# Performance work log

Measured on AMD Instinct MI355X. Metric: run time of the kernel, lower is better.

## Reference

```python
import jax, jax.numpy as jnp
import numpy as np

NUM_HEADS = 16
DIM_MODEL = 1024
DIM_K = DIM_MODEL // NUM_HEADS
B, S = 2, 2048


def _linear_params(key, d_in, d_out):
    kw, kb = jax.random.split(key)
    bound = 1.0 / np.sqrt(d_in)
    W = jax.random.uniform(kw, (d_out, d_in), jnp.float32, -bound, bound)
    b = jax.random.uniform(kb, (d_out,), jnp.float32, -bound, bound)
    return W, b


def setup_inputs() -> dict:
    key = jax.random.key(0)
    ks = jax.random.split(key, 7)
    Q_in = jax.random.normal(ks[0], (B, S, DIM_MODEL), jnp.float32)
    K_in = jax.random.normal(ks[1], (B, S, DIM_MODEL), jnp.float32)
    V_in = jax.random.normal(ks[2], (B, S, DIM_MODEL), jnp.float32)
    Wq, bq = _linear_params(ks[3], DIM_MODEL, DIM_MODEL)
    Wk, bk = _linear_params(ks[4], DIM_MODEL, DIM_MODEL)
    Wv, bv = _linear_params(ks[5], DIM_MODEL, DIM_MODEL)
    Wo, bo = _linear_params(ks[6], DIM_MODEL, DIM_MODEL)
    return {"Q_in": Q_in, "K_in": K_in, "V_in": V_in,
            "Wq": Wq, "bq": bq, "Wk": Wk, "bk": bk,
            "Wv": Wv, "bv": bv, "Wo": Wo, "bo": bo}


def reference(Q_in, K_in, V_in, Wq, bq, Wk, bk, Wv, bv, Wo, bo):
    # QKV projections (nn.Linear: x @ W.T + b)
    Q = Q_in @ Wq.T + bq
    K = K_in @ Wk.T + bk
    V = V_in @ Wv.T + bv
    # [B, S, D] -> [B, H, S, dk]
    def split_heads(x):
        return x.reshape(B, S, NUM_HEADS, DIM_K).transpose(0, 2, 1, 3)
    Qh, Kh, Vh = split_heads(Q), split_heads(K), split_heads(V)
    # Scaled dot-product attention
    scale = 1.0 / np.sqrt(DIM_K)
    scores = jnp.einsum('bhqd,bhkd->bhqk', Qh, Kh) * scale  # [B,H,S,S]
    attn = jax.nn.softmax(scores, axis=-1)
    out = jnp.einsum('bhqk,bhkd->bhqd', attn, Vh)  # [B,H,S,dk]
    # Merge heads -> [B, S, D]
    out = out.transpose(0, 2, 1, 3).reshape(B, S, DIM_MODEL)
    return out @ Wo.T + bo
```

## Files before the change

kernel.cpp:

```cpp
#include <hip/hip_runtime.h>
#include <stdint.h>

#define BB 2
#define SS 2048
#define DD 1024
#define HH 16
#define DKK 64
#define MT (BB*SS)

#define GSTRIDE 40

#define QSCALE 0.18033688011112042f

using short8  = __attribute__((ext_vector_type(8))) short;
using floatx4 = __attribute__((ext_vector_type(4))) float;
using u16x4   = __attribute__((ext_vector_type(4))) unsigned short;
typedef unsigned short u16;

__device__ __forceinline__ float ex2(float x) { return __builtin_amdgcn_exp2f(x); }

__device__ __forceinline__ u16 f2b(float f) {
  union { float f; unsigned u; } v; v.f = f;
  return (u16)((v.u + 0x7FFFu + ((v.u >> 16) & 1u)) >> 16);
}
__device__ __forceinline__ unsigned cvt_pk_bf16(float lo, float hi) {
  unsigned r;
  asm("v_cvt_pk_bf16_f32 %0, %1, %2" : "=v"(r) : "v"(lo), "v"(hi));
  return r;
}
__device__ __forceinline__ void pack16(const float4* p, short8& lo, short8& hi) {
  float4 x0 = p[0], x1 = p[1], x2 = p[2], x3 = p[3];
  lo[0]=(short)f2b(x0.x); lo[1]=(short)f2b(x0.y); lo[2]=(short)f2b(x0.z); lo[3]=(short)f2b(x0.w);
  lo[4]=(short)f2b(x1.x); lo[5]=(short)f2b(x1.y); lo[6]=(short)f2b(x1.z); lo[7]=(short)f2b(x1.w);
  hi[0]=(short)f2b(x2.x); hi[1]=(short)f2b(x2.y); hi[2]=(short)f2b(x2.z); hi[3]=(short)f2b(x2.w);
  hi[4]=(short)f2b(x3.x); hi[5]=(short)f2b(x3.y); hi[6]=(short)f2b(x3.z); hi[7]=(short)f2b(x3.w);
}
__device__ __forceinline__ void gload16(const u16* g, u16* l) {
  __builtin_amdgcn_global_load_lds(
      (const __attribute__((address_space(1))) void*)g,
      (__attribute__((address_space(3))) void*)l, 16, 0, 0);
}

__global__ __launch_bounds__(256) void cast_all(
    const float* __restrict__ Qin, const float* __restrict__ Kin,
    const float* __restrict__ Vin, const float* __restrict__ Wq,
    const float* __restrict__ Wk,  const float* __restrict__ Wv,
    const float* __restrict__ Wo,
    u16* __restrict__ cQ, u16* __restrict__ cK, u16* __restrict__ cV,
    u16* __restrict__ cWq, u16* __restrict__ cWk, u16* __restrict__ cWv,
    u16* __restrict__ cWo)
{
  const int y = blockIdx.y;
  if (y >= 3 && blockIdx.x >= (DD*DD/8/256)) return;
  const float* s; u16* d;
  switch (y) {
    case 0: s = Qin; d = cQ;  break;
    case 1: s = Kin; d = cK;  break;
    case 2: s = Vin; d = cV;  break;
    case 3: s = Wq;  d = cWq; break;
    case 4: s = Wk;  d = cWk; break;
    case 5: s = Wv;  d = cWv; break;
    default: s = Wo; d = cWo; break;
  }
  const size_t g = (size_t)blockIdx.x * 256 + threadIdx.x;
  float4 x0 = ((const float4*)s)[g*2], x1 = ((const float4*)s)[g*2+1];
  short8 lo;
  lo[0]=(short)f2b(x0.x); lo[1]=(short)f2b(x0.y); lo[2]=(short)f2b(x0.z); lo[3]=(short)f2b(x0.w);
  lo[4]=(short)f2b(x1.x); lo[5]=(short)f2b(x1.y); lo[6]=(short)f2b(x1.z); lo[7]=(short)f2b(x1.w);
  ((short8*)d)[g] = lo;
}
__global__ __launch_bounds__(256) void cast_w3(
    const float* __restrict__ w0, const float* __restrict__ w1,
    const float* __restrict__ w2, u16* __restrict__ o)
{
  const float* s = (blockIdx.y == 0) ? w0 : (blockIdx.y == 1) ? w1 : w2;
  u16* d = o + (size_t)blockIdx.y * (DD * DD);
  const size_t g = (size_t)blockIdx.x * 256 + threadIdx.x;
  float4 x0 = ((const float4*)s)[g*2], x1 = ((const float4*)s)[g*2+1];
  short8 lo;
  lo[0]=(short)f2b(x0.x); lo[1]=(short)f2b(x0.y); lo[2]=(short)f2b(x0.z); lo[3]=(short)f2b(x0.w);
  lo[4]=(short)f2b(x1.x); lo[5]=(short)f2b(x1.y); lo[6]=(short)f2b(x1.z); lo[7]=(short)f2b(x1.w);
  ((short8*)d)[g] = lo;
}

template<bool OUT_F32>
__device__ __forceinline__ void gemm_async(
    const u16* __restrict__ A, const u16* __restrict__ W,
    const float* __restrict__ bias, void* __restrict__ Cv,
    const int K, const int N, const int m0, const int n0, const float scale)
{
  __shared__ __align__(16) u16 sA[128*64];
  __shared__ __align__(16) u16 sB[128*64];

  const int tid  = threadIdx.x;
  const int wave = tid >> 6;
  const int lane = tid & 63;
  const int quad = lane >> 4;
  const int lr   = lane & 15;
  const int wm   = wave >> 1;
  const int wn   = wave & 1;
  const int srow = lane >> 3;
  const int swz  = (((lane & 7) ^ ((srow & 1) << 2)) << 3);

  floatx4 acc[4][4];
#pragma unroll
  for (int i = 0; i < 4; ++i)
#pragma unroll
    for (int j = 0; j < 4; ++j) acc[i][j] = (floatx4){0.f, 0.f, 0.f, 0.f};

  const u16* pA[4]; const u16* pW[4];
#pragma unroll
  for (int c = 0; c < 4; ++c) {
    const int row = (wave + c*4) * 8 + srow;
    pA[c] = A + (size_t)(m0 + row) * K + swz;
    pW[c] = W + (size_t)(n0 + row) * K + swz;
  }

  const int nk = K >> 6;
  for (int kt = 0; kt < nk; ++kt) {
    const int k0 = kt << 6;
#pragma unroll
    for (int c = 0; c < 4; ++c) {
      gload16(pA[c] + k0, sA + (wave + c*4) * 512);
      gload16(pW[c] + k0, sB + (wave + c*4) * 512);
    }
    __syncthreads();

#pragma unroll
    for (int h2 = 0; h2 < 2; ++h2) {
      const int csel = (quad << 3) + ((h2 ^ (lr & 1)) << 5);
      short8 af[4], bf[4];
#pragma unroll
      for (int t = 0; t < 4; ++t) {
        af[t] = *(const short8*)(sA + (wm*64 + t*16 + lr)*64 + csel);
        bf[t] = *(const short8*)(sB + (wn*64 + t*16 + lr)*64 + csel);
      }
#pragma unroll
      for (int i = 0; i < 4; ++i)
#pragma unroll
        for (int j = 0; j < 4; ++j)
          acc[i][j] = __builtin_amdgcn_mfma_f32_16x16x32_bf16(af[i], bf[j], acc[i][j], 0, 0, 0);
    }
    __syncthreads();
  }

#pragma unroll
  for (int i = 0; i < 4; ++i) {
    const int mb = m0 + wm*64 + i*16 + quad*4;
#pragma unroll
    for (int j = 0; j < 4; ++j) {
      const int n = n0 + wn*64 + j*16 + lr;
      const float bsv = bias[n];
#pragma unroll
      for (int r = 0; r < 4; ++r) {
        const size_t idx = (size_t)(mb + r) * N + n;
        const float v = (acc[i][j][r] + bsv) * scale;
        if (OUT_F32) ((float*)Cv)[idx] = v;
        else         ((u16*)Cv)[idx]   = f2b(v);
      }
    }
  }
}

__global__ __launch_bounds__(256, 3) void gemm_qkv_async(
    const u16* __restrict__ cQ, const u16* __restrict__ cK, const u16* __restrict__ cV,
    const u16* __restrict__ cWq, const u16* __restrict__ cWk, const u16* __restrict__ cWv,
    const float* __restrict__ bq, const float* __restrict__ bk, const float* __restrict__ bv,
    u16* __restrict__ oQ, u16* __restrict__ oK, u16* __restrict__ oV)
{
  const int bid = blockIdx.x;
  const int xcd = bid & 7;
  const int j   = bid >> 3;
  const int mat = j >> 5;
  const int r   = j & 31;
  const int m0  = ((xcd << 2) + (r >> 3)) * 128;
  const int n0  = (r & 7) * 128;
  const u16* A; const u16* W; const float* bias; u16* C;
  if (mat == 0)      { A = cQ; W = cWq; bias = bq; C = oQ; }
  else if (mat == 1) { A = cK; W = cWk; bias = bk; C = oK; }
  else               { A = cV; W = cWv; bias = bv; C = oV; }
  const float scale = (mat == 0) ? QSCALE : 1.0f;
  gemm_async<false>(A, W, bias, C, DD, DD, m0, n0, scale);
}

__global__ __launch_bounds__(256, 3) void gemm_out_async(
    const u16* __restrict__ A, const u16* __restrict__ cWo,
    const float* __restrict__ bias, float* __restrict__ C)
{
  const int bid = blockIdx.x;
  const int xcd = bid & 7;
  const int j   = bid >> 3;
  const int m0  = ((xcd << 2) + (j >> 3)) * 128;
  const int n0  = (j & 7) * 128;
  gemm_async<true>(A, cWo, bias, C, DD, DD, m0, n0, 1.0f);
}

template<bool A_BF16, bool W_BF16, bool OUT_F32>
__device__ __forceinline__ void gemm_core(
    const void* __restrict__ A, const void* __restrict__ W,
    const float* __restrict__ bias, void* __restrict__ Cv,
    const int K, const int N, const int m0, const int n0, const float scale)
{
  __shared__ __align__(16) u16 sA[128*GSTRIDE];
  __shared__ __align__(16) u16 sB[128*GSTRIDE];

  const int tid  = threadIdx.x;
  const int wave = tid >> 6;
  const int lane = tid & 63;
  const int quad = lane >> 4;
  const int lr   = lane & 15;
  const int wm   = wave >> 1;
  const int wn   = wave & 1;
  const int srow = tid >> 1;
  const int scol = (tid & 1) * 16;

  floatx4 acc[4][4];
#pragma unroll
  for (int i = 0; i < 4; ++i)
#pragma unroll
    for (int j = 0; j < 4; ++j) acc[i][j] = (floatx4){0.f, 0.f, 0.f, 0.f};

  const size_t offA = (size_t)(m0 + srow) * K + scol;
  const size_t offW = (size_t)(n0 + srow) * K + scol;

  const int nk = K >> 5;
  for (int kt = 0; kt < nk; ++kt) {
    const int k0 = kt << 5;
    short8 a0, a1, b0, b1;
    if (A_BF16) {
      const u16* p = (const u16*)A + offA + k0;
      a0 = *(const short8*)p; a1 = *(const short8*)(p + 8);
    } else {
      pack16((const float4*)((const float*)A + offA + k0), a0, a1);
    }
    if (W_BF16) {
      const u16* p = (const u16*)W + offW + k0;
      b0 = *(const short8*)p; b1 = *(const short8*)(p + 8);
    } else {
      pack16((const float4*)((const float*)W + offW + k0), b0, b1);
    }
    __syncthreads();
    *(short8*)(sA + srow * GSTRIDE + scol)     = a0;
    *(short8*)(sA + srow * GSTRIDE + scol + 8) = a1;
    *(short8*)(sB + srow * GSTRIDE + scol)     = b0;
    *(short8*)(sB + srow * GSTRIDE + scol + 8) = b1;
    __syncthreads();

    short8 af[4], bf[4];
#pragma unroll
    for (int t = 0; t < 4; ++t) {
      af[t] = *(const short8*)(sA + (wm*64 + t*16 + lr)*GSTRIDE + quad*8);
      bf[t] = *(const short8*)(sB + (wn*64 + t*16 + lr)*GSTRIDE + quad*8);
    }
#pragma unroll
    for (int i = 0; i < 4; ++i)
#pragma unroll
      for (int j = 0; j < 4; ++j)
        acc[i][j] = __builtin_amdgcn_mfma_f32_16x16x32_bf16(af[i], bf[j], acc[i][j], 0, 0, 0);
  }

#pragma unroll
  for (int i = 0; i < 4; ++i) {
    const int mb = m0 + wm*64 + i*16 + quad*4;
#pragma unroll
    for (int j = 0; j < 4; ++j) {
      const int n = n0 + wn*64 + j*16 + lr;
      const float bsv = bias[n];
#pragma unroll
      for (int r = 0; r < 4; ++r) {
        const size_t idx = (size_t)(mb + r) * N + n;
        const float v = (acc[i][j][r] + bsv) * scale;
        if (OUT_F32) ((float*)Cv)[idx] = v;
        else         ((u16*)Cv)[idx]   = f2b(v);
      }
    }
  }
}

__global__ __launch_bounds__(256, 2) void gemm_qkv_fb(
    const float* __restrict__ Qin, const float* __restrict__ Kin, const float* __restrict__ Vin,
    const u16* __restrict__ cWq, const u16* __restrict__ cWk, const u16* __restrict__ cWv,
    const float* __restrict__ bq, const float* __restrict__ bk, const float* __restrict__ bv,
    u16* __restrict__ oQ, u16* __restrict__ oK, u16* __restrict__ oV)
{
  const int wsel = blockIdx.x >> 3;
  const int n0 = (blockIdx.x & 7) * 128;
  const int m0 = blockIdx.y * 128;
  const float* A; const u16* W; const float* bias; u16* C;
  if (wsel == 0)      { A = Qin; W = cWq; bias = bq; C = oQ; }
  else if (wsel == 1) { A = Kin; W = cWk; bias = bk; C = oK; }
  else                { A = Vin; W = cWv; bias = bv; C = oV; }
  const float scale = (wsel == 0) ? QSCALE : 1.0f;
  gemm_core<false, true, false>(A, W, bias, C, DD, DD, m0, n0, scale);
}
__global__ __launch_bounds__(256, 2) void gemm_out_fb(
    const u16* __restrict__ A, const float* __restrict__ W,
    const float* __restrict__ bias, float* __restrict__ C)
{
  gemm_core<true, false, true>((const void*)A, (const void*)W, bias, C, DD, DD,
                               blockIdx.y * 128, blockIdx.x * 128, 1.0f);
}

__global__ __launch_bounds__(256) void transpose_v(
    const u16* __restrict__ Vp, u16* __restrict__ Vt)
{
  __shared__ u16 t[64 * 65];
  const int st = blockIdx.x, h = blockIdx.y, b = blockIdx.z;

  const int r  = threadIdx.x >> 2;
  const int c0 = (threadIdx.x & 3) * 16;
  const u16* src = Vp + ((size_t)(b * SS + st * 64 + r)) * DD + h * 64 + c0;
  short8 v0 = *(const short8*)src;
  short8 v1 = *(const short8*)(src + 8);
#pragma unroll
  for (int i = 0; i < 8; ++i) {
    t[r * 65 + c0 + i]     = (u16)v0[i];
    t[r * 65 + c0 + 8 + i] = (u16)v1[i];
  }
  __syncthreads();
  union { u16 a[16]; short8 v[2]; } ob;
#pragma unroll
  for (int i = 0; i < 16; ++i) ob.a[i] = t[(c0 + i) * 65 + r];
  u16* dst = Vt + (((size_t)(b * HH + h)) * DKK + r) * SS + st * 64 + c0;
  *(short8*)dst       = ob.v[0];
  *(short8*)(dst + 8) = ob.v[1];
}

__device__ __forceinline__ int aswz(int row, int cb) {
  return (row << 7) + (cb ^ ((row & 7) << 4));
}

__global__ __launch_bounds__(256, 2) void attn(
    const u16* __restrict__ Qp, const u16* __restrict__ Kp,
    const u16* __restrict__ Vt, u16* __restrict__ O)
{
  __shared__ __align__(16) char sK[2][64 * 128];
  __shared__ __align__(16) char sV[2][64 * 128];
  __shared__ __align__(16) char sP[4][32 * 128];

  const int tid = threadIdx.x, wave = tid >> 6, lane = tid & 63;
  const int quad = lane >> 4, lr = lane & 15;

  const int flat = (blockIdx.z * 16 + blockIdx.y) * 16 + blockIdx.x;
  const int swzb = (flat & 7) * 64 + (flat >> 3);
  const int qb = swzb & 15;
  const int h  = (swzb >> 4) & 15;
  const int b  = swzb >> 8;
  const size_t vbase = ((size_t)(b * HH + h)) * DKK * SS;

  short8 qf[2][2];
#pragma unroll
  for (int g = 0; g < 2; ++g) {
    const u16* qr = Qp + ((size_t)(b * SS + qb * 128 + wave * 32 + g * 16 + lr)) * DD + h * 64 + quad * 8;
    qf[g][0] = *(const short8*)qr;
    qf[g][1] = *(const short8*)(qr + 32);
  }

  floatx4 accO[2][4];
  float m_l[2] = { -3e38f, -3e38f }, l_l[2] = { 0.f, 0.f };
#pragma unroll
  for (int g = 0; g < 2; ++g)
#pragma unroll
    for (int t = 0; t < 4; ++t) accO[g][t] = (floatx4){0.f, 0.f, 0.f, 0.f};

  const int sr = tid >> 2;
  const int ce = (tid & 3) * 16;
  const u16* kp = Kp + ((size_t)(b * SS + sr)) * DD + h * 64 + ce;
  const u16* vp = Vt + vbase + (size_t)sr * SS + ce;
  const int dk0 = aswz(sr, ce * 2), dk1 = aswz(sr, ce * 2 + 16);

  short8 rk0 = *(const short8*)kp,        rk1 = *(const short8*)(kp + 8);
  short8 rv0 = *(const short8*)vp,        rv1 = *(const short8*)(vp + 8);
  *(short8*)(sK[0] + dk0) = rk0;  *(short8*)(sK[0] + dk1) = rk1;
  *(short8*)(sV[0] + dk0) = rv0;  *(short8*)(sV[0] + dk1) = rv1;
  kp += (size_t)64 * DD; vp += 64;
  rk0 = *(const short8*)kp;  rk1 = *(const short8*)(kp + 8);
  rv0 = *(const short8*)vp;  rv1 = *(const short8*)(vp + 8);
  __syncthreads();

  const int nt = SS / 64;
  for (int kt = 0; kt < nt; ++kt) {
    const int cur = kt & 1;
    if (kt < nt - 1) {
      *(short8*)(sK[cur ^ 1] + dk0) = rk0;  *(short8*)(sK[cur ^ 1] + dk1) = rk1;
      *(short8*)(sV[cur ^ 1] + dk0) = rv0;  *(short8*)(sV[cur ^ 1] + dk1) = rv1;
    }
    if (kt < nt - 2) {
      kp += (size_t)64 * DD; vp += 64;
      rk0 = *(const short8*)kp;  rk1 = *(const short8*)(kp + 8);
      rv0 = *(const short8*)vp;  rv1 = *(const short8*)(vp + 8);
    }
    const char* sKc = sK[cur];
    const char* sVc = sV[cur];
    char* sPw = sP[wave];

    short8 kf[4][2], vf[4][2];
#pragma unroll
    for (int t = 0; t < 4; ++t) {
      const int row = t * 16 + lr;
      kf[t][0] = *(const short8*)(sKc + aswz(row, quad * 16));
      kf[t][1] = *(const short8*)(sKc + aswz(row, 64 + quad * 16));
      vf[t][0] = *(const short8*)(sVc + aswz(row, quad * 16));
      vf[t][1] = *(const short8*)(sVc + aswz(row, 64 + quad * 16));
    }

#pragma unroll
    for (int g = 0; g < 2; ++g) {
      floatx4 st[4];
      __builtin_amdgcn_s_setprio(1);
#pragma unroll
      for (int t = 0; t < 4; ++t) {
        floatx4 cc = (floatx4){0.f, 0.f, 0.f, 0.f};
        cc = __builtin_amdgcn_mfma_f32_16x16x32_bf16(kf[t][0], qf[g][0], cc, 0, 0, 0);
        cc = __builtin_amdgcn_mfma_f32_16x16x32_bf16(kf[t][1], qf[g][1], cc, 0, 0, 0);
        st[t] = cc;
      }
      __builtin_amdgcn_s_setprio(0);

      float mx = st[0][0];
#pragma unroll
      for (int t = 0; t < 4; ++t)
#pragma unroll
        for (int r = 0; r < 4; ++r) mx = fmaxf(mx, st[t][r]);
      mx = fmaxf(mx, __shfl_xor(mx, 16, 64));
      mx = fmaxf(mx, __shfl_xor(mx, 32, 64));

      if (!__all(mx - m_l[g] <= 11.54f)) {
        const float mn2 = fmaxf(m_l[g], mx);
        const float al = ex2(m_l[g] - mn2);
        m_l[g] = mn2;
        l_l[g] *= al;
        float arow[4];
#pragma unroll
        for (int r = 0; r < 4; ++r) arow[r] = __shfl(al, quad * 4 + r, 64);
#pragma unroll
        for (int t = 0; t < 4; ++t) {
          floatx4 o = accO[g][t];
          o[0] *= arow[0]; o[1] *= arow[1]; o[2] *= arow[2]; o[3] *= arow[3];
          accO[g][t] = o;
        }
      }
      const float mn = m_l[g];

      float rs = 0.f;
      u16x4 pk[4];
#pragma unroll
      for (int t = 0; t < 4; ++t) {
        const float p0 = ex2(st[t][0] - mn);
        const float p1 = ex2(st[t][1] - mn);
        const float p2 = ex2(st[t][2] - mn);
        const float p3 = ex2(st[t][3] - mn);
        rs += (p0 + p1) + (p2 + p3);
        union { unsigned u[2]; u16x4 v; } pp;
        pp.u[0] = cvt_pk_bf16(p0, p1);
        pp.u[1] = cvt_pk_bf16(p2, p3);
        pk[t] = pp.v;
      }
      l_l[g] += rs;

#pragma unroll
      for (int t = 0; t < 4; ++t)
        *(u16x4*)(sPw + aswz(g * 16 + lr, t * 32 + quad * 8)) = pk[t];

      short8 p0 = *(const short8*)(sPw + aswz(g * 16 + lr, quad * 16));
      short8 p1 = *(const short8*)(sPw + aswz(g * 16 + lr, 64 + quad * 16));
      __builtin_amdgcn_s_setprio(1);
#pragma unroll
      for (int t = 0; t < 4; ++t) {
        accO[g][t] = __builtin_amdgcn_mfma_f32_16x16x32_bf16(p0, vf[t][0], accO[g][t], 0, 0, 0);
        accO[g][t] = __builtin_amdgcn_mfma_f32_16x16x32_bf16(p1, vf[t][1], accO[g][t], 0, 0, 0);
      }
      __builtin_amdgcn_s_setprio(0);
    }

    __syncthreads();
  }

#pragma unroll
  for (int g = 0; g < 2; ++g) {
    l_l[g] += __shfl_xor(l_l[g], 16, 64);
    l_l[g] += __shfl_xor(l_l[g], 32, 64);
    float lrow[4];
#pragma unroll
    for (int r = 0; r < 4; ++r) lrow[r] = __shfl(l_l[g], quad * 4 + r, 64);
#pragma unroll
    for (int t = 0; t < 4; ++t)
#pragma unroll
      for (int r = 0; r < 4; ++r) {
        const int s = qb * 128 + wave * 32 + g * 16 + quad * 4 + r;
        const int d = h * 64 + t * 16 + lr;
        O[((size_t)(b * SS + s)) * DD + d] = f2b(accO[g][t][r] / lrow[r]);
      }
  }
}

extern "C" void kernel_launch(void* const* d_in, const int* in_sizes, int n_in,
                              void* d_out, int out_size, void* d_ws, size_t ws_size,
                              hipStream_t stream)
{
  const float* Qin = (const float*)d_in[0];
  const float* Kin = (const float*)d_in[1];
  const float* Vin = (const float*)d_in[2];
  const float* Wq  = (const float*)d_in[3];
  const float* bq  = (const float*)d_in[4];
  const float* Wk  = (const float*)d_in[5];
  const float* bk  = (const float*)d_in[6];
  const float* Wv  = (const float*)d_in[7];
  const float* bv  = (const float*)d_in[8];
  const float* Wo  = (const float*)d_in[9];
  const float* bo  = (const float*)d_in[10];
  float* out = (float*)d_out;

  const size_t TSZ = (size_t)MT * DD;
  const size_t WSZ = (size_t)DD * DD;
  dim3 blk(256);

  u16* cWq = (u16*)d_out;
  u16* cWk = cWq + WSZ;
  u16* cWv = cWk + WSZ;

  u16* pQ   = (u16*)d_ws;
  u16* pK   = pQ  + TSZ;
  u16* pV   = pK  + TSZ;
  u16* wsVt = pV  + TSZ;
  u16* wsO  = wsVt + TSZ;

  if (ws_size >= (8*TSZ + WSZ) * sizeof(u16)) {
    u16* cQ  = wsO + TSZ;
    u16* cK  = cQ  + TSZ;
    u16* cV  = cK  + TSZ;
    u16* cWo = cV  + TSZ;
    cast_all<<<dim3(TSZ/8/256, 7), blk, 0, stream>>>(
        Qin, Kin, Vin, Wq, Wk, Wv, Wo, cQ, cK, cV, cWq, cWk, cWv, cWo);
    gemm_qkv_async<<<dim3(768), blk, 0, stream>>>(
        cQ, cK, cV, cWq, cWk, cWv, bq, bk, bv, pQ, pK, pV);
    transpose_v<<<dim3(SS/64, HH, BB), blk, 0, stream>>>(pV, wsVt);
    attn<<<dim3(SS/128, HH, BB), blk, 0, stream>>>(pQ, pK, wsVt, wsO);
    gemm_out_async<<<dim3(256), blk, 0, stream>>>(wsO, cWo, bo, out);
  } else {
    cast_w3<<<dim3(WSZ/8/256, 3), blk, 0, stream>>>(Wq, Wk, Wv, cWq);
    gemm_qkv_fb<<<dim3(24, MT/128), blk, 0, stream>>>(
        Qin, Kin, Vin, cWq, cWk, cWv, bq, bk, bv, pQ, pK, pV);
    transpose_v<<<dim3(SS/64, HH, BB), blk, 0, stream>>>(pV, wsVt);
    attn<<<dim3(SS/128, HH, BB), blk, 0, stream>>>(pQ, pK, wsVt, wsO);
    gemm_out_fb<<<dim3(DD/128, MT/128), blk, 0, stream>>>(wsO, Wo, bo, out);
  }
}
```

Measured before the change: 230.4 us.

## Load K/V fragments directly from global memory, drop shared staging and barriers

```diff
diff --git a/kernel.cpp b/kernel.cpp
--- a/kernel.cpp
+++ b/kernel.cpp
@@ -334,8 +334,6 @@
     const u16* __restrict__ Qp, const u16* __restrict__ Kp,
     const u16* __restrict__ Vt, u16* __restrict__ O)
 {
-  __shared__ __align__(16) char sK[2][64 * 128];
-  __shared__ __align__(16) char sV[2][64 * 128];
   __shared__ __align__(16) char sP[4][32 * 128];
 
   const int tid = threadIdx.x, wave = tid >> 6, lane = tid & 63;
@@ -363,65 +361,61 @@
 #pragma unroll
     for (int t = 0; t < 4; ++t) accO[g][t] = (floatx4){0.f, 0.f, 0.f, 0.f};
 
-  const int sr = tid >> 2;
-  const int ce = (tid & 3) * 16;
-  const u16* kp = Kp + ((size_t)(b * SS + sr)) * DD + h * 64 + ce;
-  const u16* vp = Vt + vbase + (size_t)sr * SS + ce;
-  const int dk0 = aswz(sr, ce * 2), dk1 = aswz(sr, ce * 2 + 16);
-
-  short8 rk0 = *(const short8*)kp,        rk1 = *(const short8*)(kp + 8);
-  short8 rv0 = *(const short8*)vp,        rv1 = *(const short8*)(vp + 8);
-  *(short8*)(sK[0] + dk0) = rk0;  *(short8*)(sK[0] + dk1) = rk1;
-  *(short8*)(sV[0] + dk0) = rv0;  *(short8*)(sV[0] + dk1) = rv1;
-  kp += (size_t)64 * DD; vp += 64;
-  rk0 = *(const short8*)kp;  rk1 = *(const short8*)(kp + 8);
-  rv0 = *(const short8*)vp;  rv1 = *(const short8*)(vp + 8);
-  __syncthreads();
+  const u16* kPtr[4]; const u16* vPtr[4];
+#pragma unroll
+  for (int t = 0; t < 4; ++t) {
+    kPtr[t] = Kp + ((size_t)(b * SS + t * 16 + lr)) * DD + h * 64 + quad * 8;
+    vPtr[t] = Vt + vbase + (size_t)(t * 16 + lr) * SS + quad * 8;
+  }
+
+  short8 kf[4][2];
+#pragma unroll
+  for (int t = 0; t < 4; ++t) {
+    kf[t][0] = *(const short8*)(kPtr[t]);
+    kf[t][1] = *(const short8*)(kPtr[t] + 32);
+    kPtr[t] += (size_t)64 * DD;
+  }
 
   const int nt = SS / 64;
+  char* sPw = sP[wave];
   for (int kt = 0; kt < nt; ++kt) {
-    const int cur = kt & 1;
-    if (kt < nt - 1) {
-      *(short8*)(sK[cur ^ 1] + dk0) = rk0;  *(short8*)(sK[cur ^ 1] + dk1) = rk1;
-      *(short8*)(sV[cur ^ 1] + dk0) = rv0;  *(short8*)(sV[cur ^ 1] + dk1) = rv1;
-    }
-    if (kt < nt - 2) {
-      kp += (size_t)64 * DD; vp += 64;
-      rk0 = *(const short8*)kp;  rk1 = *(const short8*)(kp + 8);
-      rv0 = *(const short8*)vp;  rv1 = *(const short8*)(vp + 8);
-    }
-    const char* sKc = sK[cur];
-    const char* sVc = sV[cur];
-    char* sPw = sP[wave];
-
-    short8 kf[4][2], vf[4][2];
+    short8 vf[4][2];
 #pragma unroll
     for (int t = 0; t < 4; ++t) {
-      const int row = t * 16 + lr;
-      kf[t][0] = *(const short8*)(sKc + aswz(row, quad * 16));
-      kf[t][1] = *(const short8*)(sKc + aswz(row, 64 + quad * 16));
-      vf[t][0] = *(const short8*)(sVc + aswz(row, quad * 16));
-      vf[t][1] = *(const short8*)(sVc + aswz(row, 64 + quad * 16));
-    }
-
-#pragma unroll
-    for (int g = 0; g < 2; ++g) {
-      floatx4 st[4];
-      __builtin_amdgcn_s_setprio(1);
+      vf[t][0] = *(const short8*)(vPtr[t]);
+      vf[t][1] = *(const short8*)(vPtr[t] + 32);
+      vPtr[t] += 64;
+    }
+
+    floatx4 st[2][4];
+    __builtin_amdgcn_s_setprio(1);
+#pragma unroll
+    for (int g = 0; g < 2; ++g)
 #pragma unroll
       for (int t = 0; t < 4; ++t) {
         floatx4 cc = (floatx4){0.f, 0.f, 0.f, 0.f};
         cc = __builtin_amdgcn_mfma_f32_16x16x32_bf16(kf[t][0], qf[g][0], cc, 0, 0, 0);
         cc = __builtin_amdgcn_mfma_f32_16x16x32_bf16(kf[t][1], qf[g][1], cc, 0, 0, 0);
-        st[t] = cc;
-      }
-      __builtin_amdgcn_s_setprio(0);
-
-      float mx = st[0][0];
+        st[g][t] = cc;
+      }
+    __builtin_amdgcn_s_setprio(0);
+
+    if (kt < nt - 1) {
+#pragma unroll
+      for (int t = 0; t < 4; ++t) {
+        kf[t][0] = *(const short8*)(kPtr[t]);
+        kf[t][1] = *(const short8*)(kPtr[t] + 32);
+        kPtr[t] += (size_t)64 * DD;
+      }
+    }
+
+#pragma unroll
+    for (int g = 0; g < 2; ++g) {
+      float mx = st[g][0][0];
 #pragma unroll
       for (int t = 0; t < 4; ++t)
 #pragma unroll
-        for (int r = 0; r < 4; ++r) mx = fmaxf(mx, st[t][r]);
+        for (int r = 0; r < 4; ++r) mx = fmaxf(mx, st[g][t][r]);
       mx = fmaxf(mx, __shfl_xor(mx, 16, 64));
       mx = fmaxf(mx, __shfl_xor(mx, 32, 64));
 
@@ -446,10 +440,10 @@
       u16x4 pk[4];
 #pragma unroll
       for (int t = 0; t < 4; ++t) {
-        const float p0 = ex2(st[t][0] - mn);
-        const float p1 = ex2(st[t][1] - mn);
-        const float p2 = ex2(st[t][2] - mn);
-        const float p3 = ex2(st[t][3] - mn);
+        const float p0 = ex2(st[g][t][0] - mn);
+        const float p1 = ex2(st[g][t][1] - mn);
+        const float p2 = ex2(st[g][t][2] - mn);
+        const float p3 = ex2(st[g][t][3] - mn);
         rs += (p0 + p1) + (p2 + p3);
         union { unsigned u[2]; u16x4 v; } pp;
         pp.u[0] = cvt_pk_bf16(p0, p1);
@@ -472,8 +466,6 @@
       }
       __builtin_amdgcn_s_setprio(0);
     }
-
-    __syncthreads();
   }
 
 #pragma unroll
```

After: 294.0 us. +27.6%, slower.
